# Kernel optimization log

Measured on AMD Instinct MI355X. Metric: run time of the kernel, lower is better.

Reference implementation:

```python
import jax, jax.numpy as jnp
import numpy as np

N_NODES = 1000
HIDDEN = 256
IN_DIM = 128
N_EDGES = 64000


def setup_inputs() -> dict:
    key = jax.random.key(0)
    ks = jax.random.split(key, 24)
    inp = {
        "x": jax.random.normal(ks[0], (N_NODES, IN_DIM), dtype=jnp.float32),
        "edge_index": jax.random.randint(ks[1], (2, N_EDGES), 0, N_NODES, dtype=jnp.int64),
    }
    dims = [(HIDDEN, 2 * IN_DIM)] + [(HIDDEN, 2 * HIDDEN)] * 4
    for l, (dout, din) in enumerate(dims):
        s0 = 1.0 / np.sqrt(din)
        s1 = 1.0 / np.sqrt(HIDDEN)
        inp[f"w{l}_0"] = jax.random.normal(ks[2 + 4 * l], (dout, din), dtype=jnp.float32) * s0
        inp[f"b{l}_0"] = jax.random.normal(ks[3 + 4 * l], (dout,), dtype=jnp.float32) * s0
        inp[f"w{l}_1"] = jax.random.normal(ks[4 + 4 * l], (HIDDEN, HIDDEN), dtype=jnp.float32) * s1
        inp[f"b{l}_1"] = jax.random.normal(ks[5 + 4 * l], (HIDDEN,), dtype=jnp.float32) * s1
    return inp


def _edge_conv(x, src, dst, w1, b1, w2, b2):
    # gather endpoint features per edge: [E, D]
    x_i = x[dst]  # destination (edge_index[1])
    x_j = x[src]  # source (edge_index[0])
    m = jnp.concatenate([x_i, x_j - x_i], axis=-1)  # [E, 2D]
    h = jax.nn.relu(m @ w1.T + b1) @ w2.T + b2      # 2-layer MLP, [E, HIDDEN]
    # scatter-max to destination nodes (include_self=False -> empty rows = 0)
    agg = jax.ops.segment_max(h, dst, num_segments=N_NODES)
    agg = jnp.where(jnp.isneginf(agg), jnp.zeros((), agg.dtype), agg)
    return jax.nn.relu(agg)


def reference(x, edge_index, w0_0, b0_0, w0_1, b0_1, w1_0, b1_0, w1_1, b1_1,
              w2_0, b2_0, w2_1, b2_1, w3_0, b3_0, w3_1, b3_1, w4_0, b4_0, w4_1, b4_1):
    src = edge_index[0]
    dst = edge_index[1]
    params = [(w0_0, b0_0, w0_1, b0_1), (w1_0, b1_0, w1_1, b1_1),
              (w2_0, b2_0, w2_1, b2_1), (w3_0, b3_0, w3_1, b3_1),
              (w4_0, b4_0, w4_1, b4_1)]
    h = x
    for (w1, b1, w2, b2) in params:
        h = _edge_conv(h, src, dst, w1, b1, w2, b2)
    return h
```

## Files before the change

kernel.cpp:

```cpp
#include <hip/hip_runtime.h>

#define NN 1000
#define NE 64000
#define HH 256

typedef _Float16 half8 __attribute__((ext_vector_type(8)));
typedef float floatx4 __attribute__((ext_vector_type(4)));

struct PrepArgs { const float* w0[5]; const float* w1[5]; };


template <int NK>
__device__ __forceinline__ void node_tile(const float* __restrict__ X,
                                          const _Float16* __restrict__ Wn,
                                          const float* __restrict__ b0,
                                          _Float16* __restrict__ out, int bid) {
    const int Kd = NK * 32;
    int t = threadIdx.x;
    int wave = t >> 6, lane = t & 63;
    int q = lane >> 4, mn = lane & 15;
    int m0 = (bid % 63) * 16;
    int n0 = (bid / 63) * 128 + wave * 32;
    int slice = (bid / 63) * 4 + wave;
    int rr = m0 + mn;
    if (rr >= NN) rr = NN - 1;

    half8 afa[NK];
    half8 bfa[NK][2];
#pragma unroll
    for (int kk = 0; kk < NK; kk++) {
        int ka = kk * 32 + q * 8;
        const float* p = X + (size_t)rr * Kd + ka;
        floatx4 x0 = *(const floatx4*)p;
        floatx4 x1 = *(const floatx4*)(p + 4);
        half8 aa;
#pragma unroll
        for (int j = 0; j < 4; j++) { aa[j] = (_Float16)x0[j]; aa[4 + j] = (_Float16)x1[j]; }
        afa[kk] = aa;
        bfa[kk][0] = *(const half8*)(Wn + (((slice * NK + kk) * 2 + 0) * 64 + lane) * 8);
        bfa[kk][1] = *(const half8*)(Wn + (((slice * NK + kk) * 2 + 1) * 64 + lane) * 8);
    }
    floatx4 acc[2] = {};
#pragma unroll
    for (int kk = 0; kk < NK; kk++) {
        acc[0] = __builtin_amdgcn_mfma_f32_16x16x32_f16(afa[kk], bfa[kk][0], acc[0], 0, 0, 0);
        acc[1] = __builtin_amdgcn_mfma_f32_16x16x32_f16(afa[kk], bfa[kk][1], acc[1], 0, 0, 0);
    }
#pragma unroll
    for (int nt = 0; nt < 2; nt++) {
        int col = n0 + nt * 16 + mn;
        float bias = (col < 256) ? b0[col] : 0.f;
#pragma unroll
        for (int r2 = 0; r2 < 4; r2++) {
            int orow = m0 + q * 4 + r2;
            if (orow < NN)
                out[(size_t)orow * 512 + col] = (_Float16)(acc[nt][r2] + bias);
        }
    }
}

__device__ __forceinline__ void node_tile0(const float* __restrict__ X,
                                           const float* __restrict__ w0,
                                           const float* __restrict__ b0,
                                           _Float16* __restrict__ out, int bid) {
    const int NK = 4;
    const int Kd = 128;
    int t = threadIdx.x;
    int wave = t >> 6, lane = t & 63;
    int q = lane >> 4, mn = lane & 15;
    int m0 = (bid % 63) * 16;
    int n0 = (bid / 63) * 128 + wave * 32;
    int slice = (bid / 63) * 4 + wave;
    int rr = m0 + mn;
    if (rr >= NN) rr = NN - 1;

    half8 afa[NK];
    half8 bfa[NK][2];
#pragma unroll
    for (int kk = 0; kk < NK; kk++) {
        int ka = kk * 32 + q * 8;
        const float* p = X + (size_t)rr * Kd + ka;
        floatx4 x0 = *(const floatx4*)p;
        floatx4 x1 = *(const floatx4*)(p + 4);
        half8 aa;
#pragma unroll
        for (int j = 0; j < 4; j++) { aa[j] = (_Float16)x0[j]; aa[4 + j] = (_Float16)x1[j]; }
        afa[kk] = aa;
#pragma unroll
        for (int nt = 0; nt < 2; nt++) {
            int n = slice * 32 + nt * 16 + mn;
            int k = kk * 32 + q * 8;
            half8 bb;
            if (n < 256) {
                const float* pa = w0 + (size_t)n * 256 + k;
                floatx4 a0 = *(const floatx4*)pa;
                floatx4 a1 = *(const floatx4*)(pa + 4);
                floatx4 c0 = *(const floatx4*)(pa + 128);
                floatx4 c1 = *(const floatx4*)(pa + 132);
#pragma unroll
                for (int j = 0; j < 4; j++) {
                    bb[j] = (_Float16)(a0[j] - c0[j]);
                    bb[4 + j] = (_Float16)(a1[j] - c1[j]);
                }
            } else {
                const float* pb = w0 + (size_t)(n - 256) * 256 + 128 + k;
                floatx4 c0 = *(const floatx4*)pb;
                floatx4 c1 = *(const floatx4*)(pb + 4);
#pragma unroll
                for (int j = 0; j < 4; j++) {
                    bb[j] = (_Float16)c0[j];
                    bb[4 + j] = (_Float16)c1[j];
                }
            }
            bfa[kk][nt] = bb;
        }
    }
    floatx4 acc[2] = {};
#pragma unroll
    for (int kk = 0; kk < NK; kk++) {
        acc[0] = __builtin_amdgcn_mfma_f32_16x16x32_f16(afa[kk], bfa[kk][0], acc[0], 0, 0, 0);
        acc[1] = __builtin_amdgcn_mfma_f32_16x16x32_f16(afa[kk], bfa[kk][1], acc[1], 0, 0, 0);
    }
#pragma unroll
    for (int nt = 0; nt < 2; nt++) {
        int col = n0 + nt * 16 + mn;
        float bias = (col < 256) ? b0[col] : 0.f;
#pragma unroll
        for (int r2 = 0; r2 < 4; r2++) {
            int orow = m0 + q * 4 + r2;
            if (orow < NN)
                out[(size_t)orow * 512 + col] = (_Float16)(acc[nt][r2] + bias);
        }
    }
}

__global__ __launch_bounds__(256) void k_pre1(PrepArgs pa,
                                              const int* __restrict__ ei,
                                              const float* __restrict__ X,
                                              const float* __restrict__ b0_0,
                                              _Float16* __restrict__ node_ab,
                                              _Float16* wnode, _Float16* w2h,
                                              int* cnts16, int* cursor,
                                              float* agg0, float* dout) {
    int bid = blockIdx.x;
    int t = threadIdx.x;
    if (bid < 16) {
        int* my = cnts16 + bid * 1024;
        for (int i = t; i < 1024; i += 256) my[i] = 0;
        __syncthreads();
        for (int e = bid * 256 + t; e < NE; e += 16 * 256)
            atomicAdd(&my[ei[NE + e] & 1023], 1);
    } else if (bid < 16 + 252) {
        node_tile0(X, pa.w0[0], b0_0, node_ab, bid - 16);
    } else {
        int gtid = (bid - 268) * 256 + t;
        int gs = 256 * 256;
        for (int i = gtid; i < 1024; i += gs) cursor[i] = 0;
        for (int l = 1; l < 5; l++) {
            const float* w0 = pa.w0[l];
            _Float16* wn = wnode + l * 131072;
            for (int i = gtid; i < 131072; i += gs) {
                int j = i & 7;
                int lane = (i >> 3) & 63;
                int nt = (i >> 9) & 1;
                int kk = (i >> 10) & 7;
                int slice = i >> 13;
                int mn = lane & 15, q = lane >> 4;
                int n = slice * 32 + nt * 16 + mn;
                int k = kk * 32 + q * 8 + j;
                float v = (n < 256) ? (w0[n * 512 + k] - w0[n * 512 + 256 + k])
                                    : w0[(n - 256) * 512 + 256 + k];
                wn[i] = (_Float16)v;
            }
        }
        for (int l = 0; l < 5; l++) {
            const float* w1 = pa.w1[l];
            _Float16* w2 = w2h + l * 65536;
            for (int i = gtid; i < 65536; i += gs) {
                int j = i & 7;
                int lane = (i >> 3) & 63;
                int nt = (i >> 9) & 3;
                int kk = (i >> 11) & 7;
                int ws = (i >> 14) & 3;
                int mn = lane & 15, q = lane >> 4;
                int row = ws * 64 + nt * 16 + mn;
                int col = kk * 32 + q * 8 + j;
                w2[i] = (_Float16)w1[row * 256 + col];
            }
        }
        floatx4 z = {0.f, 0.f, 0.f, 0.f};
        floatx4* p4 = (floatx4*)agg0;
        for (int i = gtid; i < 4 * NN * HH / 4; i += gs) p4[i] = z;
        floatx4* o4 = (floatx4*)dout;
        for (int i = gtid; i < NN * HH / 4; i += gs) o4[i] = z;
    }
}

__global__ __launch_bounds__(256) void k_scatter2(const int* __restrict__ ei,
                                                  const int* __restrict__ cnts16,
                                                  int* __restrict__ cursor,
                                                  int* __restrict__ ssrc,
                                                  int* __restrict__ sdst) {
    __shared__ int sbase[1024];
    __shared__ int ssum[256];
    int t = threadIdx.x;
    int base = t * 4;
    int c4[4]; int sum = 0;
#pragma unroll
    for (int j = 0; j < 4; j++) {
        int c = 0;
#pragma unroll
        for (int b = 0; b < 16; b++) c += cnts16[b * 1024 + base + j];
        c4[j] = c; sum += c;
    }
    ssum[t] = sum;
    __syncthreads();
    for (int d = 1; d < 256; d <<= 1) {
        int v = (t >= d) ? ssum[t - d] : 0;
        __syncthreads();
        ssum[t] += v;
        __syncthreads();
    }
    int run = (t > 0) ? ssum[t - 1] : 0;
#pragma unroll
    for (int j = 0; j < 4; j++) { sbase[base + j] = run; run += c4[j]; }
    __syncthreads();
    for (int e = blockIdx.x * 256 + t; e < NE; e += gridDim.x * 256) {
        int s = ei[e] & 1023, d = ei[NE + e] & 1023;
        int pos = sbase[d] + atomicAdd(&cursor[d], 1);
        if (pos < NE) { ssrc[pos] = s; sdst[pos] = d; }
    }
}

__global__ __launch_bounds__(256) void k_node(const float* __restrict__ agg_in,
                                              const _Float16* __restrict__ Wn,
                                              const float* __restrict__ b0,
                                              _Float16* __restrict__ out) {
    node_tile<8>(agg_in, Wn, b0, out, blockIdx.x);
}

__device__ __forceinline__ void edge_mfma(const _Float16* __restrict__ node_ab,
                                          const int* __restrict__ ssrc,
                                          const int* __restrict__ sdst,
                                          const _Float16* __restrict__ W2,
                                          int tile, _Float16* h1, int* sd,
                                          floatx4 acc[4][4]) {
    int t = threadIdx.x;
    int e0 = tile * 64;
    int wave = t >> 6, lane = t & 63;
    int q = lane >> 4, mn = lane & 15;
    const _Float16* W2w = W2 + wave * 16384;

    if (t < 128) sd[t] = (t < 64) ? sdst[e0 + t] : ssrc[e0 + t - 64];
    __syncthreads();
    {
        int s = lane & 31;
        int rh = lane >> 5;
#pragma unroll
        for (int it = 0; it < 8; it++) {
            int row = it * 8 + wave * 2 + rh;
            int dn = sd[row], sn = sd[64 + row];
            half8 av = *(const half8*)(node_ab + (size_t)dn * 512 + s * 8);
            half8 bv = *(const half8*)(node_ab + (size_t)sn * 512 + 256 + s * 8);
            half8 hv = av + bv;
#pragma unroll
            for (int j = 0; j < 8; j++) hv[j] = hv[j] > (_Float16)0 ? hv[j] : (_Float16)0;
            int p = (s & ~7) | ((s ^ row) & 7);
            *(half8*)(&h1[row * 256 + p * 8]) = hv;
        }
    }
    __syncthreads();

#pragma unroll
    for (int kk = 0; kk < 8; kk++) {
        half8 bf[4];
#pragma unroll
        for (int nt = 0; nt < 4; nt++)
            bf[nt] = *(const half8*)(W2w + (kk * 4 + nt) * 512 + lane * 8);
        half8 af[4];
#pragma unroll
        for (int mt = 0; mt < 4; mt++) {
            int r = mt * 16 + mn;
            int c = kk * 4 + q;
            int p = (c & ~7) | ((c ^ r) & 7);
            af[mt] = *(const half8*)(&h1[r * 256 + p * 8]);
        }
#pragma unroll
        for (int mt = 0; mt < 4; mt++)
#pragma unroll
            for (int nt = 0; nt < 4; nt++)
                acc[mt][nt] = __builtin_amdgcn_mfma_f32_16x16x32_f16(af[mt], bf[nt], acc[mt][nt], 0, 0, 0);
    }
}

__global__ __launch_bounds__(256, 4) void edge_gemm2(const _Float16* __restrict__ node_ab,
                          const int* __restrict__ ssrc, const int* __restrict__ sdst,
                          const _Float16* __restrict__ W2, const float* __restrict__ b2,
                          float* __restrict__ agg) {
    __shared__ _Float16 h1[64 * 256];
    __shared__ int sd[128];
    int t = threadIdx.x;
    int wave = t >> 6, lane = t & 63;
    int q = lane >> 4, mn = lane & 15;

    floatx4 acc[4][4] = {};
    edge_mfma(node_ab, ssrc, sdst, W2, blockIdx.x, h1, sd, acc);

    __syncthreads();
#pragma unroll
    for (int nt = 0; nt < 4; nt++) {
        int col = wave * 64 + nt * 16 + mn;
        float bias = b2[col];
        int g = col >> 3, o = col & 7;
#pragma unroll
        for (int mt = 0; mt < 4; mt++) {
#pragma unroll
            for (int r2 = 0; r2 < 4; r2++) {
                int row = mt * 16 + q * 4 + r2;
                float v = acc[mt][nt][r2] + bias;
                v = v > 0.f ? v : 0.f;
                int pg = (g & ~7) | ((g ^ row) & 7);
                h1[row * 256 + pg * 8 + o] = (_Float16)v;
            }
        }
    }
    __syncthreads();

    {
        int c = t;
        int g = c >> 3, o = c & 7;
        float* aggc = agg + c;
        float m = (float)h1[g * 8 + o];
        bool sedge = true;
        int prevd = sd[0];
#pragma unroll 8
        for (int r = 1; r < 64; r++) {
            int d = sd[r];
            int pg = (g & ~7) | ((g ^ r) & 7);
            float v = (float)h1[r * 256 + pg * 8 + o];
            if (d != prevd) {
                if (sedge) {
                    if (m > 0.f)
                        atomicMax((unsigned int*)(aggc + (size_t)prevd * HH), __float_as_uint(m));
                } else {
                    if (m > 0.f)
                        aggc[(size_t)prevd * HH] = m;
                }
                m = v; sedge = false; prevd = d;
            } else {
                m = fmaxf(m, v);
            }
        }
        if (m > 0.f)
            atomicMax((unsigned int*)(aggc + (size_t)prevd * HH), __float_as_uint(m));
    }
}

__global__ __launch_bounds__(256, 4) void edge_last(
        const _Float16* __restrict__ node_ab,
        const int* __restrict__ ssrc, const int* __restrict__ sdst,
        const _Float16* __restrict__ W2, const float* __restrict__ b2,
        float* __restrict__ agg) {
    __shared__ float sf[64 * 129];
    __shared__ int sd[128];
    _Float16* h1 = (_Float16*)sf;
    int t = threadIdx.x;
    int wave = t >> 6, lane = t & 63;
    int q = lane >> 4, mn = lane & 15;

    floatx4 acc[4][4] = {};
    edge_mfma(node_ab, ssrc, sdst, W2, blockIdx.x, h1, sd, acc);

    __syncthreads();
#pragma unroll
    for (int p = 0; p < 2; p++) {
        if (p) __syncthreads();
        if ((wave >> 1) == p) {
            int lc0 = (wave & 1) * 64;
#pragma unroll
            for (int nt = 0; nt < 4; nt++) {
                int col = wave * 64 + nt * 16 + mn;
                float bias = b2[col];
                int lc = lc0 + nt * 16 + mn;
#pragma unroll
                for (int mt = 0; mt < 4; mt++) {
#pragma unroll
                    for (int r2 = 0; r2 < 4; r2++) {
                        int row = mt * 16 + q * 4 + r2;
                        float v = acc[mt][nt][r2] + bias;
                        sf[row * 129 + lc] = v > 0.f ? v : 0.f;
                    }
                }
            }
        }
        __syncthreads();
        if (t < 128) {
            float* aggc = agg + p * 128 + t;
            float m = sf[t];
            bool sedge = true;
            int prevd = sd[0];
#pragma unroll 8
            for (int r = 1; r < 64; r++) {
                int d = sd[r];
                float v = sf[r * 129 + t];
                if (d != prevd) {
                    if (sedge) {
                        if (m > 0.f)
                            atomicMax((unsigned int*)(aggc + (size_t)prevd * HH), __float_as_uint(m));
                    } else {
                        if (m > 0.f)
                            aggc[(size_t)prevd * HH] = m;
                    }
                    m = v; sedge = false; prevd = d;
                } else {
                    m = fmaxf(m, v);
                }
            }
            if (m > 0.f)
                atomicMax((unsigned int*)(aggc + (size_t)prevd * HH), __float_as_uint(m));
        }
    }
}

extern "C" void kernel_launch(void* const* d_in, const int* in_sizes, int n_in,
                              void* d_out, int out_size, void* d_ws, size_t ws_size,
                              hipStream_t stream) {
    const float* x = (const float*)d_in[0];
    const int* ei = (const int*)d_in[1];
    PrepArgs pa;
    const float* b0s[5];
    const float* b1s[5];
    for (int l = 0; l < 5; l++) {
        pa.w0[l] = (const float*)d_in[2 + 4 * l];
        b0s[l] = (const float*)d_in[3 + 4 * l];
        pa.w1[l] = (const float*)d_in[4 + 4 * l];
        b1s[l] = (const float*)d_in[5 + 4 * l];
    }

    int* ssrc = (int*)d_ws;
    int* sdst = ssrc + NE;
    int* cnts16 = sdst + NE;
    int* cursor = cnts16 + 16 * 1024;
    _Float16* node_ab = (_Float16*)(cursor + 1024);
    float* agg0 = (float*)(node_ab + 1024 * 512);
    float* agg1 = agg0 + NN * HH;
    float* agg2 = agg1 + NN * HH;
    float* agg3 = agg2 + NN * HH;
    _Float16* wnode = (_Float16*)(agg3 + NN * HH);
    _Float16* w2h = wnode + 5 * 131072;

    hipLaunchKernelGGL(k_pre1, dim3(524), dim3(256), 0, stream,
                       pa, ei, x, b0s[0], node_ab, wnode, w2h,
                       cnts16, cursor, agg0, (float*)d_out);
    hipLaunchKernelGGL(k_scatter2, dim3(NE / 256), dim3(256), 0, stream,
                       ei, cnts16, cursor, ssrc, sdst);

    float* aggs[4] = {agg0, agg1, agg2, agg3};
    for (int l = 0; l < 4; l++) {
        hipLaunchKernelGGL(edge_gemm2, dim3(NE / 64), dim3(256), 0, stream,
                           node_ab, ssrc, sdst, w2h + (size_t)l * 65536, b1s[l], aggs[l]);
        hipLaunchKernelGGL(k_node, dim3(252), dim3(256), 0, stream,
                           aggs[l], wnode + (size_t)(l + 1) * 131072, b0s[l + 1], node_ab);
    }
    hipLaunchKernelGGL(edge_last, dim3(NE / 64), dim3(256), 0, stream,
                       node_ab, ssrc, sdst, w2h + (size_t)4 * 65536, b1s[4],
                       (float*)d_out);
}
```

Baseline: 237.5 us.

## Tile edges by destination-node chunks and reduce max in registers

The sort kernel now also builds a table of per-destination chunks of at most 64 edges, so each edge-GEMM block works on edges sharing one destination node. That node's feature row is loaded once per block, and the segment max is done with register and cross-lane shuffle reductions instead of an LDS write-back and a serial per-column scan. Each block then issues one store or atomicMax per column. The grid grows to 2048 blocks, many of them partially filled or empty, which adds padded MFMA work and more block launches. The two edge kernels are merged into one used for all five layers.

```diff
diff --git a/kernel.cpp b/kernel.cpp
--- a/kernel.cpp
+++ b/kernel.cpp
@@ -200,9 +200,10 @@
                                                   const int* __restrict__ cnts16,
                                                   int* __restrict__ cursor,
                                                   int* __restrict__ ssrc,
-                                                  int* __restrict__ sdst) {
+                                                  int4* __restrict__ table) {
     __shared__ int sbase[1024];
     __shared__ int ssum[256];
+    __shared__ int schk[256];
     int t = threadIdx.x;
     int base = t * 4;
     int c4[4]; int sum = 0;
@@ -214,21 +215,41 @@
         c4[j] = c; sum += c;
     }
     ssum[t] = sum;
+    int ch4[4]; int csum = 0;
+#pragma unroll
+    for (int j = 0; j < 4; j++) { ch4[j] = (c4[j] + 63) >> 6; csum += ch4[j]; }
+    schk[t] = csum;
     __syncthreads();
     for (int d = 1; d < 256; d <<= 1) {
-        int v = (t >= d) ? ssum[t - d] : 0;
+        int v1 = (t >= d) ? ssum[t - d] : 0;
+        int v2 = (t >= d) ? schk[t - d] : 0;
         __syncthreads();
-        ssum[t] += v;
+        ssum[t] += v1;
+        schk[t] += v2;
         __syncthreads();
     }
     int run = (t > 0) ? ssum[t - 1] : 0;
 #pragma unroll
     for (int j = 0; j < 4; j++) { sbase[base + j] = run; run += c4[j]; }
     __syncthreads();
+    if (blockIdx.x == 0) {
+        int crun = (t > 0) ? schk[t - 1] : 0;
+#pragma unroll
+        for (int j = 0; j < 4; j++) {
+            int d = base + j, c = c4[j], st = sbase[base + j], nc = ch4[j];
+            for (int k = 0; k < nc; k++) {
+                int len = c - k * 64; if (len > 64) len = 64;
+                table[crun + k] = make_int4(d, st + k * 64, len, nc == 1 ? 1 : 0);
+            }
+            crun += nc;
+        }
+        int nch = schk[255];
+        for (int i = nch + t; i < 2048; i += 256) table[i] = make_int4(0, 0, 0, 0);
+    }
     for (int e = blockIdx.x * 256 + t; e < NE; e += gridDim.x * 256) {
         int s = ei[e] & 1023, d = ei[NE + e] & 1023;
         int pos = sbase[d] + atomicAdd(&cursor[d], 1);
-        if (pos < NE) { ssrc[pos] = s; sdst[pos] = d; }
+        if (pos < NE) ssrc[pos] = s;
     }
 }
 
@@ -239,38 +260,47 @@
     node_tile<8>(agg_in, Wn, b0, out, blockIdx.x);
 }
 
-__device__ __forceinline__ void edge_mfma(const _Float16* __restrict__ node_ab,
-                                          const int* __restrict__ ssrc,
-                                          const int* __restrict__ sdst,
-                                          const _Float16* __restrict__ W2,
-                                          int tile, _Float16* h1, int* sd,
-                                          floatx4 acc[4][4]) {
-    int t = threadIdx.x;
-    int e0 = tile * 64;
+__global__ __launch_bounds__(256, 4) void edge_gemm3(const _Float16* __restrict__ node_ab,
+                          const int* __restrict__ ssrc,
+                          const int4* __restrict__ table,
+                          const _Float16* __restrict__ W2,
+                          const float* __restrict__ b2,
+                          float* __restrict__ agg) {
+    __shared__ _Float16 h1[64 * 256];
+    __shared__ int ssd[64];
+    int4 ck = table[blockIdx.x];
+    int len = ck.z;
+    if (len == 0) return;
+    int dst = ck.x, start = ck.y, sole = ck.w;
+    int t = threadIdx.x;
     int wave = t >> 6, lane = t & 63;
     int q = lane >> 4, mn = lane & 15;
     const _Float16* W2w = W2 + wave * 16384;
 
-    if (t < 128) sd[t] = (t < 64) ? sdst[e0 + t] : ssrc[e0 + t - 64];
+    if (t < 64) ssd[t] = (t < len) ? ssrc[start + t] : 0;
     __syncthreads();
     {
         int s = lane & 31;
         int rh = lane >> 5;
+        half8 av = *(const half8*)(node_ab + (size_t)dst * 512 + s * 8);
 #pragma unroll
         for (int it = 0; it < 8; it++) {
             int row = it * 8 + wave * 2 + rh;
-            int dn = sd[row], sn = sd[64 + row];
-            half8 av = *(const half8*)(node_ab + (size_t)dn * 512 + s * 8);
-            half8 bv = *(const half8*)(node_ab + (size_t)sn * 512 + 256 + s * 8);
-            half8 hv = av + bv;
-#pragma unroll
-            for (int j = 0; j < 8; j++) hv[j] = hv[j] > (_Float16)0 ? hv[j] : (_Float16)0;
+            half8 hv = {};
+            if (row < len) {
+                int sn = ssd[row];
+                half8 bv = *(const half8*)(node_ab + (size_t)sn * 512 + 256 + s * 8);
+                hv = av + bv;
+#pragma unroll
+                for (int j = 0; j < 8; j++) hv[j] = hv[j] > (_Float16)0 ? hv[j] : (_Float16)0;
+            }
             int p = (s & ~7) | ((s ^ row) & 7);
             *(half8*)(&h1[row * 256 + p * 8]) = hv;
         }
     }
     __syncthreads();
 
+    floatx4 acc[4][4] = {};
 #pragma unroll
     for (int kk = 0; kk < 8; kk++) {
         half8 bf[4];
@@ -291,134 +321,33 @@
             for (int nt = 0; nt < 4; nt++)
                 acc[mt][nt] = __builtin_amdgcn_mfma_f32_16x16x32_f16(af[mt], bf[nt], acc[mt][nt], 0, 0, 0);
     }
-}
-
-__global__ __launch_bounds__(256, 4) void edge_gemm2(const _Float16* __restrict__ node_ab,
-                          const int* __restrict__ ssrc, const int* __restrict__ sdst,
-                          const _Float16* __restrict__ W2, const float* __restrict__ b2,
-                          float* __restrict__ agg) {
-    __shared__ _Float16 h1[64 * 256];
-    __shared__ int sd[128];
-    int t = threadIdx.x;
-    int wave = t >> 6, lane = t & 63;
-    int q = lane >> 4, mn = lane & 15;
-
-    floatx4 acc[4][4] = {};
-    edge_mfma(node_ab, ssrc, sdst, W2, blockIdx.x, h1, sd, acc);
-
-    __syncthreads();
+
+    float m[4] = {-3.0e38f, -3.0e38f, -3.0e38f, -3.0e38f};
+#pragma unroll
+    for (int mt = 0; mt < 4; mt++) {
+#pragma unroll
+        for (int r2 = 0; r2 < 4; r2++) {
+            int row = mt * 16 + q * 4 + r2;
+            if (row < len) {
+#pragma unroll
+                for (int nt = 0; nt < 4; nt++) m[nt] = fmaxf(m[nt], acc[mt][nt][r2]);
+            }
+        }
+    }
 #pragma unroll
     for (int nt = 0; nt < 4; nt++) {
-        int col = wave * 64 + nt * 16 + mn;
-        float bias = b2[col];
-        int g = col >> 3, o = col & 7;
-#pragma unroll
-        for (int mt = 0; mt < 4; mt++) {
-#pragma unroll
-            for (int r2 = 0; r2 < 4; r2++) {
-                int row = mt * 16 + q * 4 + r2;
-                float v = acc[mt][nt][r2] + bias;
-                v = v > 0.f ? v : 0.f;
-                int pg = (g & ~7) | ((g ^ row) & 7);
-                h1[row * 256 + pg * 8 + o] = (_Float16)v;
-            }
-        }
-    }
-    __syncthreads();
-
-    {
-        int c = t;
-        int g = c >> 3, o = c & 7;
-        float* aggc = agg + c;
-        float m = (float)h1[g * 8 + o];
-        bool sedge = true;
-        int prevd = sd[0];
-#pragma unroll 8
-        for (int r = 1; r < 64; r++) {
-            int d = sd[r];
-            int pg = (g & ~7) | ((g ^ r) & 7);
-            float v = (float)h1[r * 256 + pg * 8 + o];
-            if (d != prevd) {
-                if (sedge) {
-                    if (m > 0.f)
-                        atomicMax((unsigned int*)(aggc + (size_t)prevd * HH), __float_as_uint(m));
-                } else {
-                    if (m > 0.f)
-                        aggc[(size_t)prevd * HH] = m;
-                }
-                m = v; sedge = false; prevd = d;
-            } else {
-                m = fmaxf(m, v);
-            }
-        }
-        if (m > 0.f)
-            atomicMax((unsigned int*)(aggc + (size_t)prevd * HH), __float_as_uint(m));
-    }
-}
-
-__global__ __launch_bounds__(256, 4) void edge_last(
-        const _Float16* __restrict__ node_ab,
-        const int* __restrict__ ssrc, const int* __restrict__ sdst,
-        const _Float16* __restrict__ W2, const float* __restrict__ b2,
-        float* __restrict__ agg) {
-    __shared__ float sf[64 * 129];
-    __shared__ int sd[128];
-    _Float16* h1 = (_Float16*)sf;
-    int t = threadIdx.x;
-    int wave = t >> 6, lane = t & 63;
-    int q = lane >> 4, mn = lane & 15;
-
-    floatx4 acc[4][4] = {};
-    edge_mfma(node_ab, ssrc, sdst, W2, blockIdx.x, h1, sd, acc);
-
-    __syncthreads();
-#pragma unroll
-    for (int p = 0; p < 2; p++) {
-        if (p) __syncthreads();
-        if ((wave >> 1) == p) {
-            int lc0 = (wave & 1) * 64;
-#pragma unroll
-            for (int nt = 0; nt < 4; nt++) {
-                int col = wave * 64 + nt * 16 + mn;
-                float bias = b2[col];
-                int lc = lc0 + nt * 16 + mn;
-#pragma unroll
-                for (int mt = 0; mt < 4; mt++) {
-#pragma unroll
-                    for (int r2 = 0; r2 < 4; r2++) {
-                        int row = mt * 16 + q * 4 + r2;
-                        float v = acc[mt][nt][r2] + bias;
-                        sf[row * 129 + lc] = v > 0.f ? v : 0.f;
-                    }
-                }
-            }
-        }
-        __syncthreads();
-        if (t < 128) {
-            float* aggc = agg + p * 128 + t;
-            float m = sf[t];
-            bool sedge = true;
-            int prevd = sd[0];
-#pragma unroll 8
-            for (int r = 1; r < 64; r++) {
-                int d = sd[r];
-                float v = sf[r * 129 + t];
-                if (d != prevd) {
-                    if (sedge) {
-                        if (m > 0.f)
-                            atomicMax((unsigned int*)(aggc + (size_t)prevd * HH), __float_as_uint(m));
-                    } else {
-                        if (m > 0.f)
-                            aggc[(size_t)prevd * HH] = m;
-                    }
-                    m = v; sedge = false; prevd = d;
-                } else {
-                    m = fmaxf(m, v);
-                }
-            }
-            if (m > 0.f)
-                atomicMax((unsigned int*)(aggc + (size_t)prevd * HH), __float_as_uint(m));
-        }
+        m[nt] = fmaxf(m[nt], __shfl_xor(m[nt], 16, 64));
+        m[nt] = fmaxf(m[nt], __shfl_xor(m[nt], 32, 64));
+    }
+    float v = (q == 0) ? m[0] : (q == 1) ? m[1] : (q == 2) ? m[2] : m[3];
+    int col = wave * 64 + q * 16 + mn;
+    v = v + b2[col];
+    v = v > 0.f ? v : 0.f;
+    float* p = agg + (size_t)dst * HH + col;
+    if (sole) {
+        *p = v;
+    } else if (v > 0.f) {
+        atomicMax((unsigned int*)p, __float_as_uint(v));
     }
 }
 
@@ -438,10 +367,10 @@
     }
 
     int* ssrc = (int*)d_ws;
-    int* sdst = ssrc + NE;
-    int* cnts16 = sdst + NE;
+    int* cnts16 = ssrc + NE;
     int* cursor = cnts16 + 16 * 1024;
-    _Float16* node_ab = (_Float16*)(cursor + 1024);
+    int4* table = (int4*)(cursor + 1024);
+    _Float16* node_ab = (_Float16*)(table + 2048);
     float* agg0 = (float*)(node_ab + 1024 * 512);
     float* agg1 = agg0 + NN * HH;
     float* agg2 = agg1 + NN * HH;
@@ -453,16 +382,14 @@
                        pa, ei, x, b0s[0], node_ab, wnode, w2h,
                        cnts16, cursor, agg0, (float*)d_out);
     hipLaunchKernelGGL(k_scatter2, dim3(NE / 256), dim3(256), 0, stream,
-                       ei, cnts16, cursor, ssrc, sdst);
-
-    float* aggs[4] = {agg0, agg1, agg2, agg3};
-    for (int l = 0; l < 4; l++) {
-        hipLaunchKernelGGL(edge_gemm2, dim3(NE / 64), dim3(256), 0, stream,
-                           node_ab, ssrc, sdst, w2h + (size_t)l * 65536, b1s[l], aggs[l]);
-        hipLaunchKernelGGL(k_node, dim3(252), dim3(256), 0, stream,
-                           aggs[l], wnode + (size_t)(l + 1) * 131072, b0s[l + 1], node_ab);
-    }
-    hipLaunchKernelGGL(edge_last, dim3(NE / 64), dim3(256), 0, stream,
-                       node_ab, ssrc, sdst, w2h + (size_t)4 * 65536, b1s[4],
-                       (float*)d_out);
-}
+                       ei, cnts16, cursor, ssrc, table);
+
+    float* aggs[5] = {agg0, agg1, agg2, agg3, (float*)d_out};
+    for (int l = 0; l < 5; l++) {
+        hipLaunchKernelGGL(edge_gemm3, dim3(2048), dim3(256), 0, stream,
+                           node_ab, ssrc, table, w2h + (size_t)l * 65536, b1s[l], aggs[l]);
+        if (l < 4)
+            hipLaunchKernelGGL(k_node, dim3(252), dim3(256), 0, stream,
+                               aggs[l], wnode + (size_t)(l + 1) * 131072, b0s[l + 1], node_ab);
+    }
+}
```

Measured after the change: 234.3 us, median of 2. About the same (-1.4%).
